# Kernel optimization log

Hardware: AMD Instinct MI355X
Metric: run time of the kernel (lower is better)

Reference implementation:

```python
import jax, jax.numpy as jnp
import numpy as np

N_HEADS = 32
KV_HEADS = 8
HEAD_DIM = 128
D_MODEL = 4096
CLIP_QKV = 8.0
ROPE_THETA = 500000.0


def setup_inputs() -> dict:
    key = jax.random.key(0)
    k1, k2, k3 = jax.random.split(key, 3)
    x = jax.random.normal(k1, (2, 2048, D_MODEL), dtype=jnp.float32)
    Wqkv = jax.random.normal(k2, ((KV_HEADS * 2 + N_HEADS) * HEAD_DIM, D_MODEL), dtype=jnp.float32) * (D_MODEL ** -0.5)
    Wout = jax.random.normal(k3, (D_MODEL, D_MODEL), dtype=jnp.float32) * (D_MODEL ** -0.5)
    return {"x": x, "Wqkv": Wqkv, "Wout": Wout}


def _rope(t):
    # t: [B, H, L, D]; half-split (non-traditional) RoPE, offset=0
    B, H, L, D = t.shape
    half = D // 2
    inv_freq = 1.0 / (ROPE_THETA ** (jnp.arange(0, half, dtype=jnp.float32) / half))
    angles = jnp.arange(L, dtype=jnp.float32)[:, None] * inv_freq[None, :]  # [L, half]
    cos = jnp.cos(angles)[None, None]  # [1,1,L,half]
    sin = jnp.sin(angles)[None, None]
    t1, t2 = t[..., :half], t[..., half:]
    return jnp.concatenate([t1 * cos - t2 * sin, t2 * cos + t1 * sin], axis=-1).astype(t.dtype)


def reference(x, Wqkv, Wout):
    B, L, D = x.shape
    qkv = jnp.clip(x @ Wqkv.T, -CLIP_QKV, CLIP_QKV)
    q = qkv[..., :D_MODEL]
    k = qkv[..., D_MODEL:D_MODEL + KV_HEADS * HEAD_DIM]
    v = qkv[..., D_MODEL + KV_HEADS * HEAD_DIM:]
    q = q.reshape(B, L, N_HEADS, HEAD_DIM).transpose(0, 2, 1, 3)   # [B,H,L,d]
    k = k.reshape(B, L, KV_HEADS, HEAD_DIM).transpose(0, 2, 1, 3)  # [B,Hkv,L,d]
    v = v.reshape(B, L, KV_HEADS, HEAD_DIM).transpose(0, 2, 1, 3)
    q = _rope(q)
    k = _rope(k)
    # GQA: broadcast kv heads to query heads
    rep = N_HEADS // KV_HEADS
    k = jnp.repeat(k, rep, axis=1)  # [B,H,L,d]
    v = jnp.repeat(v, rep, axis=1)
    scale = HEAD_DIM ** -0.5
    scores = jnp.einsum('bhqd,bhkd->bhqk', q, k) * scale
    causal = jnp.tril(jnp.ones((L, L), dtype=bool))
    scores = jnp.where(causal[None, None], scores, jnp.finfo(scores.dtype).min)
    probs = jax.nn.softmax(scores, axis=-1)
    out = jnp.einsum('bhqk,bhkd->bhqd', probs, v)
    out = out.transpose(0, 2, 1, 3).reshape(B, L, D_MODEL)
    return out @ Wout.T
```

## Files before the change

kernel.cpp:

```cpp
#include <hip/hip_runtime.h>
#include <hip/hip_bf16.h>
#include <math.h>

typedef __hip_bfloat16 bf16;
typedef __attribute__((ext_vector_type(8))) short bf16x8;
typedef __attribute__((ext_vector_type(4))) short bf16x4;
typedef __attribute__((ext_vector_type(4))) float f32x4;

__device__ __forceinline__ void glds16(const bf16* g, bf16* l) {
    __builtin_amdgcn_global_load_lds(
        (const __attribute__((address_space(1))) void*)g,
        (__attribute__((address_space(3))) void*)l, 16, 0, 0);
}

__global__ __launch_bounds__(256)
void convert_to_bf16(const void* __restrict__ src, bf16* __restrict__ dst, long n) {
    const unsigned short* u16 = (const unsigned short*)src;
    int lane = threadIdx.x & 63;
    unsigned short u = u16[lane * 2];
    int e = (u >> 7) & 0xFF;
    int isf32 = __popcll(__ballot(e >= 0x86)) > 4;
    long i = ((long)blockIdx.x * 256 + threadIdx.x) * 8;
    if (i >= n) return;
    if (isf32) {
        const float* s = (const float*)src;
        bf16x8 o;
        #pragma unroll
        for (int j = 0; j < 8; j++) {
            bf16 b = (bf16)s[i + j];
            o[j] = *(short*)&b;
        }
        *(bf16x8*)(dst + i) = o;
    } else {
        *(bf16x8*)(dst + i) = *(const bf16x8*)((const bf16*)src + i);
    }
}

template<bool CLIP, typename OUT>
__global__ __launch_bounds__(512, 2)
void gemm256(const bf16* __restrict__ A, const bf16* __restrict__ B,
             OUT* __restrict__ C, int M, int N, int K) {
    __shared__ __align__(16) bf16 sA[2][256 * 64];
    __shared__ __align__(16) bf16 sB[2][256 * 64];

    const int tid   = threadIdx.x;
    const int lane  = tid & 63;
    const int row16 = lane & 15;
    const int quad  = lane >> 4;
    const int wid   = tid >> 6;
    const int wr    = wid >> 2;
    const int wc    = wid & 3;

    const int nwg  = gridDim.x * gridDim.y;
    const int orig = blockIdx.y * gridDim.x + blockIdx.x;
    const int cpx  = nwg >> 3;
    const int sw   = (orig & 7) * cpx + (orig >> 3);
    const int bn   = sw % gridDim.x;
    const int bm   = sw / gridDim.x;

    const int srow   = tid >> 3;
    const int schunk = (tid & 7) ^ (srow & 7);
    const bf16* gA = A + (size_t)(bm * 256) * K + schunk * 8;
    const bf16* gB = B + (size_t)(bn * 256) * K + schunk * 8;

    #define STAGE256(u, t)                                                     \
        do {                                                                   \
            _Pragma("unroll")                                                  \
            for (int q = 0; q < 4; q++) {                                      \
                glds16(gA + (size_t)(q * 64 + srow) * K + (t) * 64,            \
                       &sA[u][0] + q * 4096 + tid * 8);                        \
                glds16(gB + (size_t)(q * 64 + srow) * K + (t) * 64,            \
                       &sB[u][0] + q * 4096 + tid * 8);                        \
            }                                                                  \
        } while (0)

    const int cx0 = ((quad) ^ (row16 & 7)) << 4;
    const int cx1 = ((4 + quad) ^ (row16 & 7)) << 4;
    const int aRowOff = (wr * 128 + row16) * 128;
    const int bRowOff = (wc * 64 + row16) * 128;

    f32x4 acc[8][4] = {};

    const int NT = K >> 6;
    STAGE256(0, 0);
    STAGE256(1, 1);

    for (int t = 0; t < NT; t++) {
        const int cur = t & 1;
        if (t + 1 < NT) {
            asm volatile("s_waitcnt vmcnt(8)" ::: "memory");
        } else {
            asm volatile("s_waitcnt vmcnt(0)" ::: "memory");
        }
        __builtin_amdgcn_s_barrier();
        __builtin_amdgcn_sched_barrier(0);

        const char* aRd = (const char*)(&sA[cur][0]) + aRowOff;
        const char* bRd = (const char*)(&sB[cur][0]) + bRowOff;

        bf16x8 af0[8], bf0[4];
        #pragma unroll
        for (int i = 0; i < 8; i++)
            af0[i] = *(const bf16x8*)(aRd + i * 2048 + cx0);
        #pragma unroll
        for (int j = 0; j < 4; j++)
            bf0[j] = *(const bf16x8*)(bRd + j * 2048 + cx0);
        asm volatile("s_waitcnt lgkmcnt(0)" ::: "memory");
        __builtin_amdgcn_sched_barrier(0);
        __builtin_amdgcn_s_setprio(1);
        #pragma unroll
        for (int i = 0; i < 8; i++)
            #pragma unroll
            for (int j = 0; j < 4; j++)
                acc[i][j] = __builtin_amdgcn_mfma_f32_16x16x32_bf16(
                    af0[i], bf0[j], acc[i][j], 0, 0, 0);
        __builtin_amdgcn_s_setprio(0);
        __builtin_amdgcn_sched_barrier(0);

        bf16x8 af1[8], bf1[4];
        #pragma unroll
        for (int i = 0; i < 8; i++)
            af1[i] = *(const bf16x8*)(aRd + i * 2048 + cx1);
        #pragma unroll
        for (int j = 0; j < 4; j++)
            bf1[j] = *(const bf16x8*)(bRd + j * 2048 + cx1);
        asm volatile("s_waitcnt lgkmcnt(0)" ::: "memory");
        __builtin_amdgcn_sched_barrier(0);
        __builtin_amdgcn_s_barrier();
        if (t + 2 < NT) STAGE256(cur, t + 2);

        __builtin_amdgcn_s_setprio(1);
        #pragma unroll
        for (int i = 0; i < 8; i++)
            #pragma unroll
            for (int j = 0; j < 4; j++)
                acc[i][j] = __builtin_amdgcn_mfma_f32_16x16x32_bf16(
                    af1[i], bf1[j], acc[i][j], 0, 0, 0);
        __builtin_amdgcn_s_setprio(0);
    }
    #undef STAGE256

    #pragma unroll
    for (int i = 0; i < 8; i++) {
        #pragma unroll
        for (int j = 0; j < 4; j++) {
            #pragma unroll
            for (int v = 0; v < 4; v++) {
                float val = acc[i][j][v];
                if (CLIP) val = fminf(fmaxf(val, -8.0f), 8.0f);
                int grow = bm * 256 + wr * 128 + i * 16 + quad * 4 + v;
                int gcol = bn * 256 + wc * 64 + j * 16 + row16;
                C[(size_t)grow * N + gcol] = (OUT)val;
            }
        }
    }
}

__global__ __launch_bounds__(256)
void rope_reorder(const bf16* __restrict__ qkv, bf16* __restrict__ Q,
                  bf16* __restrict__ Kd, bf16* __restrict__ VT) {
    const int token = blockIdx.y;
    const int slot  = blockIdx.x * 4 + (threadIdx.x >> 6);
    const int lane  = threadIdx.x & 63;
    const int b = token >> 11, l = token & 2047;
    const bf16* src = qkv + (size_t)token * 6144 + slot * 128;
    if (slot < 40) {
        float x1 = __bfloat162float(src[lane]);
        float x2 = __bfloat162float(src[lane + 64]);
        float inv_freq = powf(500000.0f, -(float)lane * (1.0f / 64.0f));
        float ang = (float)l * inv_freq;
        float s, c;
        sincosf(ang, &s, &c);
        float o1 = x1 * c - x2 * s;
        float o2 = x2 * c + x1 * s;
        bf16* dst;
        if (slot < 32) dst = Q  + ((size_t)(b * 32 + slot)        * 2048 + l) * 128;
        else           dst = Kd + ((size_t)(b * 8  + (slot - 32)) * 2048 + l) * 128;
        dst[lane]      = (bf16)o1;
        dst[lane + 64] = (bf16)o2;
    } else {
        bf16* dst = VT + (size_t)(b * 8 + (slot - 40)) * 128 * 2048 + l;
        dst[(size_t)lane * 2048]        = src[lane];
        dst[(size_t)(lane + 64) * 2048] = src[lane + 64];
    }
}

#define SP_STR 72

__global__ __launch_bounds__(256, 3)
void attn_kernel(const bf16* __restrict__ Q, const bf16* __restrict__ K,
                 const bf16* __restrict__ V, bf16* __restrict__ Oout) {
    const int qt = 31 - blockIdx.x;
    const int bh = blockIdx.y;
    const int b = bh >> 5, h = bh & 31;
    const int kh = h >> 2;
    const bf16* Qp = Q + ((size_t)(b * 32 + h) * 2048 + qt * 64) * 128;
    const bf16* Kp = K + (size_t)(b * 8 + kh) * 2048 * 128;
    const bf16* Vp = V + (size_t)(b * 8 + kh) * 128 * 2048;

    __shared__ __align__(16) bf16 sK[64 * 128];
    __shared__ __align__(16) bf16 sV[128 * 64];
    __shared__ __align__(16) bf16 sP[4 * 16 * SP_STR];

    const int tid = threadIdx.x, lane = tid & 63, wave = tid >> 6;
    const int row = lane & 15, quad = lane >> 4;
    const int rx  = (row & 7) << 4;
    char* sKb = (char*)sK;
    char* sVb = (char*)sV;

    const int krow = tid >> 4;
    const int kc8  = (tid & 15) ^ (krow & 7);
    const int vrow = tid >> 3;
    const int vc8  = (tid & 7) ^ (vrow & 7);
    const int ldst = tid * 16;

    bf16x8 aq[4];
    #pragma unroll
    for (int kk = 0; kk < 4; kk++)
        aq[kk] = *(const bf16x8*)(Qp + (size_t)(wave * 16 + row) * 128 + (kk * 4 + quad) * 8);

    bf16x8 kpf[4], vpf[4];
    #pragma unroll
    for (int j = 0; j < 4; j++) {
        kpf[j] = *(const bf16x8*)(Kp + (size_t)(j * 16 + krow) * 128 + kc8 * 8);
        vpf[j] = *(const bf16x8*)(Vp + (size_t)(j * 32 + vrow) * 2048 + vc8 * 8);
    }
    #pragma unroll
    for (int j = 0; j < 4; j++) {
        *(bf16x8*)(sKb + ldst + j * 4096) = kpf[j];
        *(bf16x8*)(sVb + ldst + j * 4096) = vpf[j];
    }
    __syncthreads();

    float pm = -1e30f, pl = 0.0f;
    f32x4 o_acc[8] = {};
    const float scale = 0.08838834764831845f;

    for (int jj = 0; jj <= qt; jj++) {
        if (jj < qt) {
            #pragma unroll
            for (int j = 0; j < 4; j++) {
                kpf[j] = *(const bf16x8*)(Kp + (size_t)((jj + 1) * 64 + j * 16 + krow) * 128 + kc8 * 8);
                vpf[j] = *(const bf16x8*)(Vp + (size_t)(j * 32 + vrow) * 2048 + (jj + 1) * 64 + vc8 * 8);
            }
        }

        f32x4 s_acc[4] = {};
        __builtin_amdgcn_s_setprio(1);
        #pragma unroll
        for (int nt = 0; nt < 4; nt++) {
            #pragma unroll
            for (int kk = 0; kk < 4; kk++) {
                bf16x8 bk = *(const bf16x8*)(sKb + (nt * 16 + row) * 256
                                             + (((kk * 4 + quad) * 16) ^ rx));
                s_acc[nt] = __builtin_amdgcn_mfma_f32_16x16x32_bf16(
                    bk, aq[kk], s_acc[nt], 0, 0, 0);
            }
        }
        __builtin_amdgcn_s_setprio(0);

        #pragma unroll
        for (int nt = 0; nt < 4; nt++) {
            #pragma unroll
            for (int v = 0; v < 4; v++) {
                float s = s_acc[nt][v] * scale;
                if (jj == qt) {
                    int kpos = nt * 16 + quad * 4 + v;
                    int qrow = wave * 16 + row;
                    if (kpos > qrow) s = -1e30f;
                }
                s_acc[nt][v] = s;
            }
        }
        float m_loc = s_acc[0][0];
        #pragma unroll
        for (int nt = 0; nt < 4; nt++)
            #pragma unroll
            for (int v = 0; v < 4; v++)
                m_loc = fmaxf(m_loc, s_acc[nt][v]);
        m_loc = fmaxf(m_loc, __shfl_xor(m_loc, 16, 64));
        m_loc = fmaxf(m_loc, __shfl_xor(m_loc, 32, 64));

        if (!__all(m_loc - pm <= 8.0f)) {
            float mn = fmaxf(pm, m_loc);
            float al = __expf(pm - mn);
            pm = mn;
            pl *= al;
            float al_q[4];
            #pragma unroll
            for (int v = 0; v < 4; v++)
                al_q[v] = __shfl(al, quad * 4 + v, 64);
            #pragma unroll
            for (int dt = 0; dt < 8; dt++)
                #pragma unroll
                for (int v = 0; v < 4; v++)
                    o_acc[dt][v] *= al_q[v];
        }

        float rs = 0.0f;
        #pragma unroll
        for (int nt = 0; nt < 4; nt++) {
            bf16x4 pw;
            #pragma unroll
            for (int v = 0; v < 4; v++) {
                float p = __expf(s_acc[nt][v] - pm);
                rs += p;
                bf16 pb = (bf16)p;
                pw[v] = *(short*)&pb;
            }
            *(bf16x4*)(sP + (wave * 16 + row) * SP_STR + nt * 16 + quad * 4) = pw;
        }
        rs += __shfl_xor(rs, 16, 64);
        rs += __shfl_xor(rs, 32, 64);
        pl += rs;

        __builtin_amdgcn_s_setprio(1);
        #pragma unroll
        for (int kk = 0; kk < 2; kk++) {
            bf16x8 pa = *(const bf16x8*)(sP + (wave * 16 + row) * SP_STR + (kk * 4 + quad) * 8);
            #pragma unroll
            for (int dt = 0; dt < 8; dt++) {
                bf16x8 vb = *(const bf16x8*)(sVb + (dt * 16 + row) * 128
                                             + (((kk * 4 + quad) * 16) ^ rx));
                o_acc[dt] = __builtin_amdgcn_mfma_f32_16x16x32_bf16(
                    pa, vb, o_acc[dt], 0, 0, 0);
            }
        }
        __builtin_amdgcn_s_setprio(0);

        if (jj < qt) {
            __syncthreads();
            #pragma unroll
            for (int j = 0; j < 4; j++) {
                *(bf16x8*)(sKb + ldst + j * 4096) = kpf[j];
                *(bf16x8*)(sVb + ldst + j * 4096) = vpf[j];
            }
            __syncthreads();
        }
    }

    float pl_q[4];
    #pragma unroll
    for (int v = 0; v < 4; v++)
        pl_q[v] = __shfl(pl, quad * 4 + v, 64);
    const int token = b * 2048 + qt * 64 + wave * 16;
    #pragma unroll
    for (int dt = 0; dt < 8; dt++) {
        #pragma unroll
        for (int v = 0; v < 4; v++) {
            float o = o_acc[dt][v] / pl_q[v];
            int trow = token + quad * 4 + v;
            Oout[(size_t)trow * 4096 + h * 128 + dt * 16 + row] = (bf16)o;
        }
    }
}

extern "C" void kernel_launch(void* const* d_in, const int* in_sizes, int n_in,
                              void* d_out, int out_size, void* d_ws, size_t ws_size,
                              hipStream_t stream) {
    float* out = (float*)d_out;

    const size_t MB = 1024 * 1024;
    char* ws = (char*)d_ws;
    bf16* xb    = (bf16*)(ws);
    bf16* Wqkvb = (bf16*)(ws + 32 * MB);
    bf16* qkv   = (bf16*)(ws + 80 * MB);
    bf16* Qb    = (bf16*)(ws + 32 * MB);
    bf16* Kb    = (bf16*)(ws + 64 * MB);
    bf16* VTb   = (bf16*)(ws + 72 * MB);
    bf16* Woutb = (bf16*)(ws + 80 * MB);
    bf16* attn  = xb;

    convert_to_bf16<<<8192,  256, 0, stream>>>(d_in[0], xb,    16777216L);
    convert_to_bf16<<<12288, 256, 0, stream>>>(d_in[1], Wqkvb, 25165824L);
    gemm256<true, bf16><<<dim3(24, 16), 512, 0, stream>>>(xb, Wqkvb, qkv, 4096, 6144, 4096);
    rope_reorder<<<dim3(12, 4096), 256, 0, stream>>>(qkv, Qb, Kb, VTb);
    convert_to_bf16<<<8192,  256, 0, stream>>>(d_in[2], Woutb, 16777216L);
    attn_kernel<<<dim3(32, 64), 256, 0, stream>>>(Qb, Kb, VTb, attn);
    gemm256<false, float><<<dim3(16, 16), 512, 0, stream>>>(attn, Woutb, out, 4096, 4096, 4096);
}
```

Before: 845.4 us.

## Template GEMM tile width and restructure LDS read/barrier pipeline

Makes the GEMM's N-tile width a template parameter and uses a 256x192 tile for the QKV projection, giving 512 workgroups instead of 384, which better fills the 256 CUs. The main loop is also reordered: both K-half fragment loads are issued up front with partial lgkmcnt waits, and the vmcnt wait plus barrier move to the end of the iteration. This lets LDS reads overlap the first MFMA batch. The trade-off is higher register pressure from holding both fragment sets, and a narrower B tile that lowers arithmetic intensity.

```diff
diff --git a/kernel.cpp b/kernel.cpp
--- a/kernel.cpp
+++ b/kernel.cpp
@@ -36,12 +36,14 @@
     }
 }
 
-template<bool CLIP, typename OUT>
+template<int BN, bool CLIP, typename OUT>
 __global__ __launch_bounds__(512, 2)
 void gemm256(const bf16* __restrict__ A, const bf16* __restrict__ B,
              OUT* __restrict__ C, int M, int N, int K) {
+    constexpr int NB = BN / 64;
+    constexpr int WN = BN / 4;
     __shared__ __align__(16) bf16 sA[2][256 * 64];
-    __shared__ __align__(16) bf16 sB[2][256 * 64];
+    __shared__ __align__(16) bf16 sB[2][BN * 64];
 
     const int tid   = threadIdx.x;
     const int lane  = tid & 63;
@@ -61,95 +63,106 @@
     const int srow   = tid >> 3;
     const int schunk = (tid & 7) ^ (srow & 7);
     const bf16* gA = A + (size_t)(bm * 256) * K + schunk * 8;
-    const bf16* gB = B + (size_t)(bn * 256) * K + schunk * 8;
-
-    #define STAGE256(u, t)                                                     \
-        do {                                                                   \
-            _Pragma("unroll")                                                  \
-            for (int q = 0; q < 4; q++) {                                      \
-                glds16(gA + (size_t)(q * 64 + srow) * K + (t) * 64,            \
-                       &sA[u][0] + q * 4096 + tid * 8);                        \
-                glds16(gB + (size_t)(q * 64 + srow) * K + (t) * 64,            \
-                       &sB[u][0] + q * 4096 + tid * 8);                        \
-            }                                                                  \
-        } while (0)
+    const bf16* gB = B + (size_t)(bn * BN) * K + schunk * 8;
+
+    auto STAGE = [&](int u, int t) {
+        #pragma unroll
+        for (int q = 0; q < 4; q++)
+            glds16(gA + (size_t)(q * 64 + srow) * K + t * 64,
+                   &sA[u][0] + q * 4096 + tid * 8);
+        #pragma unroll
+        for (int q = 0; q < NB; q++)
+            glds16(gB + (size_t)(q * 64 + srow) * K + t * 64,
+                   &sB[u][0] + q * 4096 + tid * 8);
+    };
 
     const int cx0 = ((quad) ^ (row16 & 7)) << 4;
     const int cx1 = ((4 + quad) ^ (row16 & 7)) << 4;
     const int aRowOff = (wr * 128 + row16) * 128;
-    const int bRowOff = (wc * 64 + row16) * 128;
-
-    f32x4 acc[8][4] = {};
+    const int bRowOff = (wc * WN + row16) * 128;
+
+    f32x4 acc[8][NB] = {};
 
     const int NT = K >> 6;
-    STAGE256(0, 0);
-    STAGE256(1, 1);
+    STAGE(0, 0);
+    STAGE(1, 1);
+    if constexpr (NB == 4) asm volatile("s_waitcnt vmcnt(8)" ::: "memory");
+    else                   asm volatile("s_waitcnt vmcnt(7)" ::: "memory");
+    __builtin_amdgcn_sched_barrier(0);
+    __builtin_amdgcn_s_barrier();
 
     for (int t = 0; t < NT; t++) {
         const int cur = t & 1;
-        if (t + 1 < NT) {
-            asm volatile("s_waitcnt vmcnt(8)" ::: "memory");
-        } else {
-            asm volatile("s_waitcnt vmcnt(0)" ::: "memory");
-        }
-        __builtin_amdgcn_s_barrier();
-        __builtin_amdgcn_sched_barrier(0);
-
         const char* aRd = (const char*)(&sA[cur][0]) + aRowOff;
         const char* bRd = (const char*)(&sB[cur][0]) + bRowOff;
 
-        bf16x8 af0[8], bf0[4];
+        bf16x8 af0[8], bf0[NB], af1[8], bf1[NB];
         #pragma unroll
         for (int i = 0; i < 8; i++)
             af0[i] = *(const bf16x8*)(aRd + i * 2048 + cx0);
         #pragma unroll
-        for (int j = 0; j < 4; j++)
+        for (int j = 0; j < NB; j++)
             bf0[j] = *(const bf16x8*)(bRd + j * 2048 + cx0);
-        asm volatile("s_waitcnt lgkmcnt(0)" ::: "memory");
-        __builtin_amdgcn_sched_barrier(0);
+        __builtin_amdgcn_sched_barrier(0);
+        #pragma unroll
+        for (int i = 0; i < 8; i++)
+            af1[i] = *(const bf16x8*)(aRd + i * 2048 + cx1);
+        #pragma unroll
+        for (int j = 0; j < NB; j++)
+            bf1[j] = *(const bf16x8*)(bRd + j * 2048 + cx1);
+        __builtin_amdgcn_sched_barrier(0);
+
+        if constexpr (NB == 4) asm volatile("s_waitcnt lgkmcnt(12)" ::: "memory");
+        else                   asm volatile("s_waitcnt lgkmcnt(11)" ::: "memory");
+        __builtin_amdgcn_sched_barrier(0);
+
         __builtin_amdgcn_s_setprio(1);
         #pragma unroll
         for (int i = 0; i < 8; i++)
             #pragma unroll
-            for (int j = 0; j < 4; j++)
+            for (int j = 0; j < NB; j++)
                 acc[i][j] = __builtin_amdgcn_mfma_f32_16x16x32_bf16(
                     af0[i], bf0[j], acc[i][j], 0, 0, 0);
         __builtin_amdgcn_s_setprio(0);
         __builtin_amdgcn_sched_barrier(0);
 
-        bf16x8 af1[8], bf1[4];
+        asm volatile("s_waitcnt lgkmcnt(0)" ::: "memory");
+        __builtin_amdgcn_sched_barrier(0);
+        __builtin_amdgcn_s_barrier();
+
+        if (t + 2 < NT) STAGE(cur, t + 2);
+        __builtin_amdgcn_sched_barrier(0);
+
+        __builtin_amdgcn_s_setprio(1);
         #pragma unroll
         for (int i = 0; i < 8; i++)
-            af1[i] = *(const bf16x8*)(aRd + i * 2048 + cx1);
-        #pragma unroll
-        for (int j = 0; j < 4; j++)
-            bf1[j] = *(const bf16x8*)(bRd + j * 2048 + cx1);
-        asm volatile("s_waitcnt lgkmcnt(0)" ::: "memory");
-        __builtin_amdgcn_sched_barrier(0);
-        __builtin_amdgcn_s_barrier();
-        if (t + 2 < NT) STAGE256(cur, t + 2);
-
-        __builtin_amdgcn_s_setprio(1);
-        #pragma unroll
-        for (int i = 0; i < 8; i++)
-            #pragma unroll
-            for (int j = 0; j < 4; j++)
+            #pragma unroll
+            for (int j = 0; j < NB; j++)
                 acc[i][j] = __builtin_amdgcn_mfma_f32_16x16x32_bf16(
                     af1[i], bf1[j], acc[i][j], 0, 0, 0);
         __builtin_amdgcn_s_setprio(0);
-    }
-    #undef STAGE256
+        __builtin_amdgcn_sched_barrier(0);
+
+        if (t + 2 < NT) {
+            if constexpr (NB == 4) asm volatile("s_waitcnt vmcnt(8)" ::: "memory");
+            else                   asm volatile("s_waitcnt vmcnt(7)" ::: "memory");
+        } else {
+            asm volatile("s_waitcnt vmcnt(0)" ::: "memory");
+        }
+        __builtin_amdgcn_sched_barrier(0);
+        __builtin_amdgcn_s_barrier();
+    }
 
     #pragma unroll
     for (int i = 0; i < 8; i++) {
         #pragma unroll
-        for (int j = 0; j < 4; j++) {
+        for (int j = 0; j < NB; j++) {
             #pragma unroll
             for (int v = 0; v < 4; v++) {
                 float val = acc[i][j][v];
                 if (CLIP) val = fminf(fmaxf(val, -8.0f), 8.0f);
                 int grow = bm * 256 + wr * 128 + i * 16 + quad * 4 + v;
-                int gcol = bn * 256 + wc * 64 + j * 16 + row16;
+                int gcol = bn * BN + wc * WN + j * 16 + row16;
                 C[(size_t)grow * N + gcol] = (OUT)val;
             }
         }
@@ -373,9 +386,9 @@
 
     convert_to_bf16<<<8192,  256, 0, stream>>>(d_in[0], xb,    16777216L);
     convert_to_bf16<<<12288, 256, 0, stream>>>(d_in[1], Wqkvb, 25165824L);
-    gemm256<true, bf16><<<dim3(24, 16), 512, 0, stream>>>(xb, Wqkvb, qkv, 4096, 6144, 4096);
+    gemm256<192, true, bf16><<<dim3(32, 16), 512, 0, stream>>>(xb, Wqkvb, qkv, 4096, 6144, 4096);
     rope_reorder<<<dim3(12, 4096), 256, 0, stream>>>(qkv, Qb, Kb, VTb);
     convert_to_bf16<<<8192,  256, 0, stream>>>(d_in[2], Woutb, 16777216L);
     attn_kernel<<<dim3(32, 64), 256, 0, stream>>>(Qb, Kb, VTb, attn);
-    gemm256<false, float><<<dim3(16, 16), 512, 0, stream>>>(attn, Woutb, out, 4096, 4096, 4096);
-}
+    gemm256<256, false, float><<<dim3(16, 16), 512, 0, stream>>>(attn, Woutb, out, 4096, 4096, 4096);
+}
```

Result: faster. 788.6 us (-6.7%).
